# Optimization experiments

Measured on AMD Instinct MI355X. Metric: run time of the kernel, lower is better.

## Reference

```python
import jax, jax.numpy as jnp
import numpy as np

NUM_GROUPS = 16
EPS = 1e-6


def setup_inputs() -> dict:
    key = jax.random.key(0)
    ks = jax.random.split(key, 6)
    b, c, t, h, w = 2, 256, 4, 32, 32
    x = jax.random.normal(ks[0], (b, c, t, h, w), dtype=jnp.float32)
    scale = 0.02
    return {
        "x": x,
        "gamma": jnp.ones((c,), jnp.float32),
        "beta": jnp.zeros((c,), jnp.float32),
        "wq": jax.random.normal(ks[1], (c, c), jnp.float32) * scale,
        "bq": jnp.zeros((c,), jnp.float32),
        "wk": jax.random.normal(ks[2], (c, c), jnp.float32) * scale,
        "bk": jnp.zeros((c,), jnp.float32),
        "wv": jax.random.normal(ks[3], (c, c), jnp.float32) * scale,
        "bv": jnp.zeros((c,), jnp.float32),
        "wp": jax.random.normal(ks[4], (c, c), jnp.float32) * scale,
        "bp": jnp.zeros((c,), jnp.float32),
    }


def _group_norm(x, gamma, beta):
    b, c, t, h, w = x.shape
    xg = x.reshape(b, NUM_GROUPS, -1)  # [b, G, (c/G)*t*h*w]
    mu = jnp.mean(xg, axis=2, keepdims=True)
    var = jnp.var(xg, axis=2, keepdims=True)
    xn = ((xg - mu) * jax.lax.rsqrt(var + EPS)).reshape(b, c, t, h, w)
    return xn * gamma[None, :, None, None, None] + beta[None, :, None, None, None]


def reference(x, gamma, beta, wq, bq, wk, bk, wv, bv, wp, bp):
    b, c, t, h, w = x.shape
    n = t * h * w
    hn = _group_norm(x, gamma, beta).reshape(b, c, n)  # [b, c, n]
    # 1x1x1 conv == channel matmul
    q = jnp.einsum("oc,bcn->bon", wq, hn) + bq[None, :, None]
    k = jnp.einsum("oc,bcn->bon", wk, hn) + bk[None, :, None]
    v = jnp.einsum("oc,bcn->bon", wv, hn) + bv[None, :, None]
    # scores[b, i, j] = sum_c q[b,c,i] k[b,c,j] / sqrt(c)
    scores = jnp.einsum("bci,bcj->bij", q, k) * (float(c) ** -0.5)
    attn = jax.nn.softmax(scores, axis=2)  # [b, n, n]
    # h_[b, c, i] = sum_j v[b,c,j] attn[b,i,j]
    ho = jnp.einsum("bcj,bij->bci", v, attn)
    out = jnp.einsum("oc,bcn->bon", wp, ho) + bp[None, :, None]
    return x + out.reshape(b, c, t, h, w)
```

## Files before the change

### kernel.cpp

```cpp
#include <hip/hip_runtime.h>
#include <hip/hip_bf16.h>

#define NB 2
#define NC 256
#define NN 4096
#define NG 16
#define GSZ (16*NN)
#define SPLIT 4
#define SCL 0.09014205f

typedef __attribute__((ext_vector_type(8))) short bf16x8;
typedef __attribute__((ext_vector_type(4))) float f32x4;
typedef __attribute__((ext_vector_type(8))) unsigned short u16x8;

static __device__ __forceinline__ unsigned short f2b(float f) {
    union { float f; unsigned u; } x; x.f = f;
    unsigned r = x.u + 0x7fffu + ((x.u >> 16) & 1u);
    return (unsigned short)(r >> 16);
}
static __device__ __forceinline__ float b2f(unsigned short u) {
    union { unsigned u; float f; } x; x.u = ((unsigned)u) << 16;
    return x.f;
}
static __device__ __forceinline__ void glds16(const void* g, void* l) {
    __builtin_amdgcn_global_load_lds(
        (const __attribute__((address_space(1))) unsigned int*)g,
        (__attribute__((address_space(3))) unsigned int*)l, 16, 0, 0);
}

__global__ void k_wcvt(const float* __restrict__ wq, const float* __restrict__ wk,
                       const float* __restrict__ wv, const float* __restrict__ wp,
                       unsigned short* __restrict__ dst) {
    int idx = (blockIdx.x * 256 + threadIdx.x) * 4;
    int which = idx >> 16, off = idx & 65535;
    const float* s = (which == 0) ? wq : (which == 1) ? wk : (which == 2) ? wv : wp;
    float4 v = *(const float4*)(s + off);
    dst[idx + 0] = f2b(v.x);
    dst[idx + 1] = f2b(v.y);
    dst[idx + 2] = f2b(v.z);
    dst[idx + 3] = f2b(v.w);
}

__global__ void k_stats(const float* __restrict__ x, float* __restrict__ stats) {
    int bg = blockIdx.x >> 3, seg = blockIdx.x & 7;
    const float4* p = (const float4*)(x + (size_t)bg * GSZ + (size_t)seg * (GSZ / 8));
    float s1 = 0.f, s2 = 0.f;
    for (int k = threadIdx.x; k < GSZ / 8 / 4; k += 256) {
        float4 v = p[k];
        s1 += v.x + v.y + v.z + v.w;
        s2 += v.x*v.x + v.y*v.y + v.z*v.z + v.w*v.w;
    }
    #pragma unroll
    for (int m = 1; m < 64; m <<= 1) { s1 += __shfl_xor(s1, m); s2 += __shfl_xor(s2, m); }
    __shared__ float r1[4], r2[4];
    int w = threadIdx.x >> 6;
    if ((threadIdx.x & 63) == 0) { r1[w] = s1; r2[w] = s2; }
    __syncthreads();
    if (threadIdx.x == 0) {
        float a = 0.f, b = 0.f;
        #pragma unroll
        for (int i = 0; i < 4; i++) { a += r1[i]; b += r2[i]; }
        atomicAdd(&stats[bg * 2], a);
        atomicAdd(&stats[bg * 2 + 1], b);
    }
}

__global__ void k_norm_t(const float* __restrict__ x, const float* __restrict__ gamma,
                         const float* __restrict__ beta, const float* __restrict__ stats,
                         unsigned short* __restrict__ hn_t) {
    __shared__ unsigned short tile[64][66];
    int n0 = blockIdx.x * 64, c0 = blockIdx.y * 64, b = blockIdx.z;
    int cc = threadIdx.x >> 2, part = threadIdx.x & 3;
    int c = c0 + cc;
    float s1 = stats[(b * NG + (c >> 4)) * 2];
    float s2 = stats[(b * NG + (c >> 4)) * 2 + 1];
    float mean = s1 * (1.f / (float)GSZ);
    float var  = s2 * (1.f / (float)GSZ) - mean * mean;
    float rstd = rsqrtf(var + 1e-6f);
    float sc = rstd * gamma[c];
    float sh = beta[c] - mean * sc;
    const float4* row = (const float4*)(x + ((size_t)b * NC + c) * NN + n0);
    #pragma unroll
    for (int q = 0; q < 4; q++) {
        int f4 = part * 4 + q;
        float4 v = row[f4];
        tile[cc][f4*4+0] = f2b(v.x * sc + sh);
        tile[cc][f4*4+1] = f2b(v.y * sc + sh);
        tile[cc][f4*4+2] = f2b(v.z * sc + sh);
        tile[cc][f4*4+3] = f2b(v.w * sc + sh);
    }
    __syncthreads();
    int nn = threadIdx.x >> 2;
    u16x8 o0, o1;
    #pragma unroll
    for (int e = 0; e < 8; e++) { o0[e] = tile[part*16 + e][nn]; o1[e] = tile[part*16 + 8 + e][nn]; }
    unsigned short* dst = hn_t + ((size_t)b * NN + n0 + nn) * NC + c0 + part * 16;
    *(u16x8*)dst = o0;
    *(u16x8*)(dst + 8) = o1;
}

__global__ __launch_bounds__(256, 2) void k_qkv(
        const unsigned short* __restrict__ hn_t, const unsigned short* __restrict__ wb,
        const float* __restrict__ bq, const float* __restrict__ bk, const float* __restrict__ bv,
        unsigned short* __restrict__ q_t, unsigned short* __restrict__ k_t,
        unsigned short* __restrict__ v_cm) {
    int i0 = blockIdx.x * 64, which = blockIdx.y, b = blockIdx.z;
    int lane = threadIdx.x & 63, w = threadIdx.x >> 6;
    const unsigned short* W = wb + which * 65536;
    const float* bias = (which == 0) ? bq : (which == 1) ? bk : bv;
    if (which < 2) {
        const unsigned short* arow =
            hn_t + ((size_t)b * NN + i0 + w * 16 + (lane & 15)) * NC + ((lane >> 4) * 8);
        f32x4 acc[16];
        #pragma unroll
        for (int t = 0; t < 16; t++) acc[t] = (f32x4){0.f, 0.f, 0.f, 0.f};
        #pragma unroll
        for (int kk = 0; kk < 8; kk++) {
            bf16x8 af = *(const bf16x8*)(arow + kk * 32);
            const unsigned short* bbase = W + (size_t)(lane & 15) * NC + kk * 32 + ((lane >> 4) * 8);
            #pragma unroll
            for (int ot = 0; ot < 16; ot++) {
                bf16x8 bf_ = *(const bf16x8*)(bbase + (size_t)ot * 16 * NC);
                acc[ot] = __builtin_amdgcn_mfma_f32_16x16x32_bf16(af, bf_, acc[ot], 0, 0, 0);
            }
        }
        unsigned short* dst = ((which == 0) ? q_t : k_t) + (size_t)b * NN * NC;
        #pragma unroll
        for (int ot = 0; ot < 16; ot++) {
            float bv_ = bias[ot * 16 + (lane & 15)];
            #pragma unroll
            for (int r = 0; r < 4; r++) {
                int i = i0 + w * 16 + (lane >> 4) * 4 + r;
                dst[(size_t)i * NC + ot * 16 + (lane & 15)] = f2b(acc[ot][r] + bv_);
            }
        }
    } else {
        f32x4 acc[4][4];
        #pragma unroll
        for (int mt = 0; mt < 4; mt++)
            #pragma unroll
            for (int nt = 0; nt < 4; nt++) acc[mt][nt] = (f32x4){0.f, 0.f, 0.f, 0.f};
        #pragma unroll
        for (int kk = 0; kk < 8; kk++) {
            bf16x8 bfr[4];
            #pragma unroll
            for (int nt = 0; nt < 4; nt++)
                bfr[nt] = *(const bf16x8*)(hn_t + ((size_t)b * NN + i0 + nt * 16 + (lane & 15)) * NC
                                           + kk * 32 + ((lane >> 4) * 8));
            #pragma unroll
            for (int mt = 0; mt < 4; mt++) {
                bf16x8 af = *(const bf16x8*)(W + (size_t)(w * 64 + mt * 16 + (lane & 15)) * NC
                                             + kk * 32 + ((lane >> 4) * 8));
                #pragma unroll
                for (int nt = 0; nt < 4; nt++)
                    acc[mt][nt] = __builtin_amdgcn_mfma_f32_16x16x32_bf16(af, bfr[nt], acc[mt][nt], 0, 0, 0);
            }
        }
        #pragma unroll
        for (int mt = 0; mt < 4; mt++) {
            #pragma unroll
            for (int r = 0; r < 4; r++) {
                int o = w * 64 + mt * 16 + (lane >> 4) * 4 + r;
                float bv_ = bias[o];
                #pragma unroll
                for (int nt = 0; nt < 4; nt++) {
                    int i = i0 + nt * 16 + (lane & 15);
                    v_cm[(size_t)b * NC * NN + (size_t)o * NN + i] = f2b(acc[mt][nt][r] + bv_);
                }
            }
        }
    }
}

__global__ __launch_bounds__(512, 2) void k_attn(
        const unsigned short* __restrict__ q_t, const unsigned short* __restrict__ k_t,
        const unsigned short* __restrict__ v_cm,
        unsigned short* __restrict__ po, float* __restrict__ ml) {
    __shared__ __attribute__((aligned(16))) unsigned short Ks[2][16384];
    __shared__ __attribute__((aligned(16))) unsigned short Vs[2][16384];
    __shared__ __attribute__((aligned(16))) unsigned short Ps[8][1024];
    int d = blockIdx.x;
    int g = d & 7, xb = d >> 3;
    int sp = g & 3, b = g >> 2;
    int i0 = xb * 128;
    int lane = threadIdx.x & 63, w = threadIdx.x >> 6;
    size_t bO = (size_t)b * NN * NC;
    bf16x8 qf[8];
    {
        const unsigned short* qrow =
            q_t + bO + (size_t)(i0 + w * 16 + (lane & 15)) * NC + ((lane >> 4) * 8);
        #pragma unroll
        for (int kk = 0; kk < 8; kk++) qf[kk] = *(const bf16x8*)(qrow + kk * 32);
    }
    int j0b = sp * 1024;
    const char* gpk[4];
    const char* gpv[4];
    {
        const char* kbase = (const char*)(k_t + bO);
        const char* vbase = (const char*)(v_cm + bO);
        #pragma unroll
        for (int r = 0; r < 4; r++) {
            int jr = r * 16 + w * 2 + (lane >> 5);
            int cb = (lane & 31) * 16;
            gpk[r] = kbase + (size_t)(j0b + jr) * 512 + (cb ^ ((jr & 7) << 4));
            int cr = r * 64 + w * 8 + (lane >> 3);
            int jb = (lane & 7) * 16;
            gpv[r] = vbase + (size_t)cr * 8192 + (size_t)j0b * 2 + (jb ^ ((cr & 7) << 4));
        }
    }
    f32x4 o[16];
    #pragma unroll
    for (int t = 0; t < 16; t++) o[t] = (f32x4){0.f, 0.f, 0.f, 0.f};
    float m[4], l[4];
    #pragma unroll
    for (int r = 0; r < 4; r++) { m[r] = -1e30f; l[r] = 0.f; }
    #pragma unroll
    for (int r = 0; r < 4; r++) {
        glds16(gpk[r], (char*)&Ks[0][0] + w * 1024 + r * 8192);
        glds16(gpv[r], (char*)&Vs[0][0] + w * 1024 + r * 8192);
    }
    __syncthreads();
    int cur = 0;
    #pragma unroll 1
    for (int t = 0; t < 16; ++t) {
        if (t < 15) {
            #pragma unroll
            for (int r = 0; r < 4; r++) { gpk[r] += 32768; gpv[r] += 128; }
            int nb = cur ^ 1;
            #pragma unroll
            for (int r = 0; r < 4; r++) {
                glds16(gpk[r], (char*)&Ks[nb][0] + w * 1024 + r * 8192);
                glds16(gpv[r], (char*)&Vs[nb][0] + w * 1024 + r * 8192);
            }
        }
        const char* KsB = (const char*)&Ks[cur][0];
        const char* VsB = (const char*)&Vs[cur][0];
        f32x4 s[4];
        #pragma unroll
        for (int tt = 0; tt < 4; tt++) s[tt] = (f32x4){0.f, 0.f, 0.f, 0.f};
        #pragma unroll
        for (int kk = 0; kk < 8; kk++) {
            #pragma unroll
            for (int tt = 0; tt < 4; tt++) {
                unsigned off = ((unsigned)((tt * 16 + (lane & 15)) * 512 + kk * 64 + ((lane >> 4) * 16)))
                               ^ (((unsigned)(lane & 7)) << 4);
                bf16x8 kf = *(const bf16x8*)(KsB + off);
                s[tt] = __builtin_amdgcn_mfma_f32_16x16x32_bf16(qf[kk], kf, s[tt], 0, 0, 0);
            }
        }
        float corr[4];
        #pragma unroll
        for (int r = 0; r < 4; r++) {
            float v0 = fmaxf(fmaxf(s[0][r], s[1][r]), fmaxf(s[2][r], s[3][r]));
            v0 = fmaxf(v0, __shfl_xor(v0, 1));
            v0 = fmaxf(v0, __shfl_xor(v0, 2));
            v0 = fmaxf(v0, __shfl_xor(v0, 4));
            v0 = fmaxf(v0, __shfl_xor(v0, 8));
            float mn = fmaxf(m[r], v0);
            corr[r] = exp2f((m[r] - mn) * SCL);
            m[r] = mn;
        }
        float rs[4] = {0.f, 0.f, 0.f, 0.f};
        #pragma unroll
        for (int tt = 0; tt < 4; tt++) {
            #pragma unroll
            for (int r = 0; r < 4; r++) {
                float p = exp2f((s[tt][r] - m[r]) * SCL);
                rs[r] += p;
                unsigned i_ = (lane >> 4) * 4 + r;
                unsigned off = ((unsigned)(i_ * 128 + (tt * 16 + (lane & 15)) * 2)) ^ ((i_ & 7) << 4);
                *(unsigned short*)((char*)&Ps[w][0] + off) = f2b(p);
            }
        }
        #pragma unroll
        for (int r = 0; r < 4; r++) {
            float v0 = rs[r];
            v0 += __shfl_xor(v0, 1); v0 += __shfl_xor(v0, 2);
            v0 += __shfl_xor(v0, 4); v0 += __shfl_xor(v0, 8);
            l[r] = l[r] * corr[r] + v0;
        }
        #pragma unroll
        for (int tt = 0; tt < 16; tt++) {
            #pragma unroll
            for (int r = 0; r < 4; r++) o[tt][r] *= corr[r];
        }
        #pragma unroll
        for (int kk = 0; kk < 2; kk++) {
            unsigned offp = ((unsigned)((lane & 15) * 128 + kk * 64 + ((lane >> 4) * 16)))
                            ^ (((unsigned)(lane & 7)) << 4);
            bf16x8 pf = *(const bf16x8*)((char*)&Ps[w][0] + offp);
            #pragma unroll
            for (int ct = 0; ct < 16; ct++) {
                unsigned offv = ((unsigned)((ct * 16 + (lane & 15)) * 128 + kk * 64 + ((lane >> 4) * 16)))
                                ^ (((unsigned)(lane & 7)) << 4);
                bf16x8 vf = *(const bf16x8*)(VsB + offv);
                o[ct] = __builtin_amdgcn_mfma_f32_16x16x32_bf16(pf, vf, o[ct], 0, 0, 0);
            }
        }
        __syncthreads();
        cur ^= 1;
    }
    unsigned short* dst = po + ((size_t)(sp * NB + b) * NN) * NC;
    #pragma unroll
    for (int ct = 0; ct < 16; ct++) {
        #pragma unroll
        for (int r = 0; r < 4; r++) {
            int i = i0 + w * 16 + (lane >> 4) * 4 + r;
            dst[(size_t)i * NC + ct * 16 + (lane & 15)] = f2b(o[ct][r]);
        }
    }
    if ((lane & 15) == 0) {
        #pragma unroll
        for (int r = 0; r < 4; r++) {
            int i = i0 + w * 16 + (lane >> 4) * 4 + r;
            size_t mi = ((size_t)(sp * NB + b) * NN + i) * 2;
            ml[mi] = m[r];
            ml[mi + 1] = l[r];
        }
    }
}

__global__ void k_winv(const float* __restrict__ ml, float* __restrict__ winv) {
    int idx = blockIdx.x * 256 + threadIdx.x;
    float mv[SPLIT], lv[SPLIT];
    float M = -1e30f;
    #pragma unroll
    for (int s = 0; s < SPLIT; s++) {
        size_t mi = ((size_t)(s * 8192 + idx)) * 2;
        mv[s] = ml[mi]; lv[s] = ml[mi + 1];
        M = fmaxf(M, mv[s]);
    }
    float den = 0.f, wg[SPLIT];
    #pragma unroll
    for (int s = 0; s < SPLIT; s++) { wg[s] = exp2f((mv[s] - M) * SCL); den += wg[s] * lv[s]; }
    float inv = 1.f / den;
    #pragma unroll
    for (int s = 0; s < SPLIT; s++) winv[s * 8192 + idx] = wg[s] * inv;
}

__global__ __launch_bounds__(256, 4) void k_proj(
        const unsigned short* __restrict__ po, const float* __restrict__ winv,
        const unsigned short* __restrict__ wp_b, const float* __restrict__ bp,
        const float* __restrict__ x, float* __restrict__ out) {
    __shared__ __attribute__((aligned(16))) unsigned short Hs[32 * 256];
    int i0 = blockIdx.x * 32, b = blockIdx.y;
    int tid = threadIdx.x, lane = tid & 63, w = tid >> 6;
    {
        int il = tid >> 3, cq = tid & 7;
        int i = i0 + il;
        float wg[SPLIT];
        #pragma unroll
        for (int s = 0; s < SPLIT; s++) wg[s] = winv[s * 8192 + b * NN + i];
        #pragma unroll
        for (int e = 0; e < 4; e++) {
            float accv[8];
            #pragma unroll
            for (int q = 0; q < 8; q++) accv[q] = 0.f;
            #pragma unroll
            for (int s = 0; s < SPLIT; s++) {
                u16x8 v = *(const u16x8*)(po + ((size_t)(s * NB + b) * NN + i) * NC + cq * 32 + e * 8);
                #pragma unroll
                for (int q = 0; q < 8; q++) accv[q] += wg[s] * b2f(v[q]);
            }
            u16x8 rv;
            #pragma unroll
            for (int q = 0; q < 8; q++) rv[q] = f2b(accv[q]);
            unsigned off = ((unsigned)(il * 512 + cq * 64 + e * 16)) ^ ((il & 7) << 4);
            *(u16x8*)((char*)Hs + off) = rv;
        }
    }
    __syncthreads();
    f32x4 acc[4][2];
    #pragma unroll
    for (int mt = 0; mt < 4; mt++)
        #pragma unroll
        for (int nt = 0; nt < 2; nt++) acc[mt][nt] = (f32x4){0.f, 0.f, 0.f, 0.f};
    #pragma unroll
    for (int kk = 0; kk < 8; kk++) {
        bf16x8 bfr[2];
        #pragma unroll
        for (int nt = 0; nt < 2; nt++) {
            unsigned off = ((unsigned)((nt * 16 + (lane & 15)) * 512 + kk * 64 + ((lane >> 4) * 16)))
                           ^ (((unsigned)(lane & 7)) << 4);
            bfr[nt] = *(const bf16x8*)((char*)Hs + off);
        }
        #pragma unroll
        for (int mt = 0; mt < 4; mt++) {
            bf16x8 af = *(const bf16x8*)(wp_b + (size_t)(w * 64 + mt * 16 + (lane & 15)) * NC
                                         + kk * 32 + ((lane >> 4) * 8));
            #pragma unroll
            for (int nt = 0; nt < 2; nt++)
                acc[mt][nt] = __builtin_amdgcn_mfma_f32_16x16x32_bf16(af, bfr[nt], acc[mt][nt], 0, 0, 0);
        }
    }
    #pragma unroll
    for (int mt = 0; mt < 4; mt++) {
        #pragma unroll
        for (int r = 0; r < 4; r++) {
            int o = w * 64 + mt * 16 + (lane >> 4) * 4 + r;
            float bv_ = bp[o];
            #pragma unroll
            for (int nt = 0; nt < 2; nt++) {
                int i = i0 + nt * 16 + (lane & 15);
                size_t idx = ((size_t)b * NC + o) * NN + i;
                out[idx] = x[idx] + acc[mt][nt][r] + bv_;
            }
        }
    }
}

extern "C" void kernel_launch(void* const* d_in, const int* in_sizes, int n_in,
                              void* d_out, int out_size, void* d_ws, size_t ws_size,
                              hipStream_t stream) {
    const float* x     = (const float*)d_in[0];
    const float* gamma = (const float*)d_in[1];
    const float* beta  = (const float*)d_in[2];
    const float* wq    = (const float*)d_in[3];
    const float* bq    = (const float*)d_in[4];
    const float* wk    = (const float*)d_in[5];
    const float* bk    = (const float*)d_in[6];
    const float* wv    = (const float*)d_in[7];
    const float* bv    = (const float*)d_in[8];
    const float* wp    = (const float*)d_in[9];
    const float* bp    = (const float*)d_in[10];
    float* out = (float*)d_out;

    char* ws = (char*)d_ws;
    const size_t SZ_T = (size_t)NB * NN * NC * 2;
    float*          stats = (float*)ws;
    unsigned short* wb    = (unsigned short*)(ws + 1024);
    unsigned short* hn_t  = (unsigned short*)(ws + 1024 + 524288);
    unsigned short* q_t   = (unsigned short*)((char*)hn_t + SZ_T);
    unsigned short* k_t   = (unsigned short*)((char*)q_t + SZ_T);
    unsigned short* v_cm  = (unsigned short*)((char*)k_t + SZ_T);
    unsigned short* po    = (unsigned short*)((char*)v_cm + SZ_T);
    float*          ml    = (float*)((char*)po + (size_t)SPLIT * SZ_T);
    float*          winv  = (float*)((char*)ml + 262144);

    hipMemsetAsync(stats, 0, 1024, stream);
    k_wcvt<<<256, 256, 0, stream>>>(wq, wk, wv, wp, wb);
    k_stats<<<256, 256, 0, stream>>>(x, stats);
    k_norm_t<<<dim3(NN / 64, NC / 64, NB), 256, 0, stream>>>(x, gamma, beta, stats, hn_t);
    k_qkv<<<dim3(NN / 64, 3, NB), 256, 0, stream>>>(hn_t, wb, bq, bk, bv, q_t, k_t, v_cm);
    k_attn<<<256, 512, 0, stream>>>(q_t, k_t, v_cm, po, ml);
    k_winv<<<32, 256, 0, stream>>>(ml, winv);
    k_proj<<<dim3(NN / 32, NB), 256, 0, stream>>>(po, winv, wb + 3 * 65536, bp, x, out);
}
```

Before: 216.0 us.

## Double query rows per attention wave, split keys 8-way, lazy softmax rescale, fuse combine

Each attention wave now handles two 16-row query tiles, so every K/V fragment read from LDS feeds twice as many MFMAs. The key range is split eight ways, which keeps 256 blocks. The online softmax only rescales the output accumulators when the running max grows past a threshold, skipping most of the per-tile correction multiplies. The separate k_winv kernel is folded into k_proj, which removes one launch, and the workspace is repacked so po aliases hn_t. The added cost is twice as many accumulator registers (risk of spills or lower occupancy) and a larger split-combine step in k_proj; s_setprio hints are also added around the MFMA sections.

```diff
diff --git a/kernel.cpp b/kernel.cpp
--- a/kernel.cpp
+++ b/kernel.cpp
@@ -6,8 +6,10 @@
 #define NN 4096
 #define NG 16
 #define GSZ (16*NN)
-#define SPLIT 4
+#define SPLIT 8
+#define JT (NN / SPLIT / 64)
 #define SCL 0.09014205f
+#define THRRAW 88.0f
 
 typedef __attribute__((ext_vector_type(8))) short bf16x8;
 typedef __attribute__((ext_vector_type(4))) float f32x4;
@@ -99,7 +101,7 @@
     *(u16x8*)(dst + 8) = o1;
 }
 
-__global__ __launch_bounds__(256, 2) void k_qkv(
+__global__ __launch_bounds__(256, 4) void k_qkv(
         const unsigned short* __restrict__ hn_t, const unsigned short* __restrict__ wb,
         const float* __restrict__ bq, const float* __restrict__ bk, const float* __restrict__ bv,
         unsigned short* __restrict__ q_t, unsigned short* __restrict__ k_t,
@@ -178,66 +180,66 @@
         unsigned short* __restrict__ po, float* __restrict__ ml) {
     __shared__ __attribute__((aligned(16))) unsigned short Ks[2][16384];
     __shared__ __attribute__((aligned(16))) unsigned short Vs[2][16384];
-    __shared__ __attribute__((aligned(16))) unsigned short Ps[8][1024];
-    int d = blockIdx.x;
-    int g = d & 7, xb = d >> 3;
-    int sp = g & 3, b = g >> 2;
-    int i0 = xb * 128;
+    __shared__ __attribute__((aligned(16))) unsigned short Ps[8][2048];
+    int bid = blockIdx.x;
+    int sp = bid & 7, b = (bid >> 3) & 1, xb = bid >> 4;
+    int i0 = xb * 256;
     int lane = threadIdx.x & 63, w = threadIdx.x >> 6;
     size_t bO = (size_t)b * NN * NC;
-    bf16x8 qf[8];
-    {
+    bf16x8 qf[2][8];
+    #pragma unroll
+    for (int h = 0; h < 2; h++) {
         const unsigned short* qrow =
-            q_t + bO + (size_t)(i0 + w * 16 + (lane & 15)) * NC + ((lane >> 4) * 8);
-        #pragma unroll
-        for (int kk = 0; kk < 8; kk++) qf[kk] = *(const bf16x8*)(qrow + kk * 32);
-    }
-    int j0b = sp * 1024;
-    const char* gpk[4];
-    const char* gpv[4];
-    {
-        const char* kbase = (const char*)(k_t + bO);
-        const char* vbase = (const char*)(v_cm + bO);
-        #pragma unroll
-        for (int r = 0; r < 4; r++) {
-            int jr = r * 16 + w * 2 + (lane >> 5);
-            int cb = (lane & 31) * 16;
-            gpk[r] = kbase + (size_t)(j0b + jr) * 512 + (cb ^ ((jr & 7) << 4));
-            int cr = r * 64 + w * 8 + (lane >> 3);
-            int jb = (lane & 7) * 16;
-            gpv[r] = vbase + (size_t)cr * 8192 + (size_t)j0b * 2 + (jb ^ ((cr & 7) << 4));
-        }
-    }
-    f32x4 o[16];
-    #pragma unroll
-    for (int t = 0; t < 16; t++) o[t] = (f32x4){0.f, 0.f, 0.f, 0.f};
-    float m[4], l[4];
-    #pragma unroll
-    for (int r = 0; r < 4; r++) { m[r] = -1e30f; l[r] = 0.f; }
+            q_t + bO + (size_t)(i0 + w * 32 + h * 16 + (lane & 15)) * NC + ((lane >> 4) * 8);
+        #pragma unroll
+        for (int kk = 0; kk < 8; kk++) qf[h][kk] = *(const bf16x8*)(qrow + kk * 32);
+    }
+    unsigned kstat[4], vstat[4];
     #pragma unroll
     for (int r = 0; r < 4; r++) {
-        glds16(gpk[r], (char*)&Ks[0][0] + w * 1024 + r * 8192);
-        glds16(gpv[r], (char*)&Vs[0][0] + w * 1024 + r * 8192);
+        int jr = r * 16 + w * 2 + (lane >> 5);
+        kstat[r] = (unsigned)(jr * 512 + (((lane & 31) * 16) ^ ((jr & 7) << 4)));
+        int cr = r * 64 + w * 8 + (lane >> 3);
+        vstat[r] = (unsigned)(cr * 8192 + (((lane & 7) * 16) ^ ((cr & 7) << 4)));
+    }
+    const char* kp = (const char*)(k_t + bO) + (size_t)sp * 262144;
+    const char* vp = (const char*)(v_cm + bO) + (size_t)sp * 1024;
+    f32x4 o[2][16];
+    #pragma unroll
+    for (int h = 0; h < 2; h++)
+        #pragma unroll
+        for (int t = 0; t < 16; t++) o[h][t] = (f32x4){0.f, 0.f, 0.f, 0.f};
+    float m[2][4], l[2][4];
+    #pragma unroll
+    for (int h = 0; h < 2; h++)
+        #pragma unroll
+        for (int r = 0; r < 4; r++) { m[h][r] = -1e30f; l[h][r] = 0.f; }
+    #pragma unroll
+    for (int r = 0; r < 4; r++) {
+        glds16(kp + kstat[r], (char*)&Ks[0][0] + w * 1024 + r * 8192);
+        glds16(vp + vstat[r], (char*)&Vs[0][0] + w * 1024 + r * 8192);
     }
     __syncthreads();
     int cur = 0;
     #pragma unroll 1
-    for (int t = 0; t < 16; ++t) {
-        if (t < 15) {
-            #pragma unroll
-            for (int r = 0; r < 4; r++) { gpk[r] += 32768; gpv[r] += 128; }
+    for (int t = 0; t < JT; ++t) {
+        if (t < JT - 1) {
+            kp += 32768; vp += 128;
             int nb = cur ^ 1;
             #pragma unroll
             for (int r = 0; r < 4; r++) {
-                glds16(gpk[r], (char*)&Ks[nb][0] + w * 1024 + r * 8192);
-                glds16(gpv[r], (char*)&Vs[nb][0] + w * 1024 + r * 8192);
+                glds16(kp + kstat[r], (char*)&Ks[nb][0] + w * 1024 + r * 8192);
+                glds16(vp + vstat[r], (char*)&Vs[nb][0] + w * 1024 + r * 8192);
             }
         }
         const char* KsB = (const char*)&Ks[cur][0];
         const char* VsB = (const char*)&Vs[cur][0];
-        f32x4 s[4];
-        #pragma unroll
-        for (int tt = 0; tt < 4; tt++) s[tt] = (f32x4){0.f, 0.f, 0.f, 0.f};
+        f32x4 s[2][4];
+        #pragma unroll
+        for (int h = 0; h < 2; h++)
+            #pragma unroll
+            for (int tt = 0; tt < 4; tt++) s[h][tt] = (f32x4){0.f, 0.f, 0.f, 0.f};
+        __builtin_amdgcn_s_setprio(1);
         #pragma unroll
         for (int kk = 0; kk < 8; kk++) {
             #pragma unroll
@@ -245,101 +247,109 @@
                 unsigned off = ((unsigned)((tt * 16 + (lane & 15)) * 512 + kk * 64 + ((lane >> 4) * 16)))
                                ^ (((unsigned)(lane & 7)) << 4);
                 bf16x8 kf = *(const bf16x8*)(KsB + off);
-                s[tt] = __builtin_amdgcn_mfma_f32_16x16x32_bf16(qf[kk], kf, s[tt], 0, 0, 0);
-            }
-        }
-        float corr[4];
-        #pragma unroll
-        for (int r = 0; r < 4; r++) {
-            float v0 = fmaxf(fmaxf(s[0][r], s[1][r]), fmaxf(s[2][r], s[3][r]));
-            v0 = fmaxf(v0, __shfl_xor(v0, 1));
-            v0 = fmaxf(v0, __shfl_xor(v0, 2));
-            v0 = fmaxf(v0, __shfl_xor(v0, 4));
-            v0 = fmaxf(v0, __shfl_xor(v0, 8));
-            float mn = fmaxf(m[r], v0);
-            corr[r] = exp2f((m[r] - mn) * SCL);
-            m[r] = mn;
-        }
-        float rs[4] = {0.f, 0.f, 0.f, 0.f};
-        #pragma unroll
-        for (int tt = 0; tt < 4; tt++) {
-            #pragma unroll
-            for (int r = 0; r < 4; r++) {
-                float p = exp2f((s[tt][r] - m[r]) * SCL);
-                rs[r] += p;
-                unsigned i_ = (lane >> 4) * 4 + r;
-                unsigned off = ((unsigned)(i_ * 128 + (tt * 16 + (lane & 15)) * 2)) ^ ((i_ & 7) << 4);
-                *(unsigned short*)((char*)&Ps[w][0] + off) = f2b(p);
-            }
-        }
-        #pragma unroll
-        for (int r = 0; r < 4; r++) {
-            float v0 = rs[r];
-            v0 += __shfl_xor(v0, 1); v0 += __shfl_xor(v0, 2);
-            v0 += __shfl_xor(v0, 4); v0 += __shfl_xor(v0, 8);
-            l[r] = l[r] * corr[r] + v0;
-        }
-        #pragma unroll
-        for (int tt = 0; tt < 16; tt++) {
-            #pragma unroll
-            for (int r = 0; r < 4; r++) o[tt][r] *= corr[r];
-        }
+                s[0][tt] = __builtin_amdgcn_mfma_f32_16x16x32_bf16(qf[0][kk], kf, s[0][tt], 0, 0, 0);
+                s[1][tt] = __builtin_amdgcn_mfma_f32_16x16x32_bf16(qf[1][kk], kf, s[1][tt], 0, 0, 0);
+            }
+        }
+        __builtin_amdgcn_s_setprio(0);
+        #pragma unroll
+        for (int h = 0; h < 2; h++) {
+            float vmax[4];
+            #pragma unroll
+            for (int r = 0; r < 4; r++) {
+                float v0 = fmaxf(fmaxf(s[h][0][r], s[h][1][r]), fmaxf(s[h][2][r], s[h][3][r]));
+                v0 = fmaxf(v0, __shfl_xor(v0, 1));
+                v0 = fmaxf(v0, __shfl_xor(v0, 2));
+                v0 = fmaxf(v0, __shfl_xor(v0, 4));
+                v0 = fmaxf(v0, __shfl_xor(v0, 8));
+                vmax[r] = v0;
+            }
+            float tmax = fmaxf(fmaxf(vmax[0] - m[h][0], vmax[1] - m[h][1]),
+                               fmaxf(vmax[2] - m[h][2], vmax[3] - m[h][3]));
+            tmax = fmaxf(tmax, __shfl_xor(tmax, 16));
+            tmax = fmaxf(tmax, __shfl_xor(tmax, 32));
+            if (tmax > THRRAW) {
+                #pragma unroll
+                for (int r = 0; r < 4; r++) {
+                    float mn = fmaxf(m[h][r], vmax[r]);
+                    float corr = exp2f((m[h][r] - mn) * SCL);
+                    m[h][r] = mn;
+                    l[h][r] *= corr;
+                    #pragma unroll
+                    for (int ct = 0; ct < 16; ct++) o[h][ct][r] *= corr;
+                }
+            }
+            float rs[4] = {0.f, 0.f, 0.f, 0.f};
+            #pragma unroll
+            for (int tt = 0; tt < 4; tt++) {
+                #pragma unroll
+                for (int r = 0; r < 4; r++) {
+                    float p = exp2f((s[h][tt][r] - m[h][r]) * SCL);
+                    rs[r] += p;
+                    unsigned i_ = (unsigned)(h * 16 + (lane >> 4) * 4 + r);
+                    unsigned off = ((unsigned)(i_ * 128 + (tt * 16 + (lane & 15)) * 2)) ^ ((i_ & 7) << 4);
+                    *(unsigned short*)((char*)&Ps[w][0] + off) = f2b(p);
+                }
+            }
+            #pragma unroll
+            for (int r = 0; r < 4; r++) {
+                float v0 = rs[r];
+                v0 += __shfl_xor(v0, 1); v0 += __shfl_xor(v0, 2);
+                v0 += __shfl_xor(v0, 4); v0 += __shfl_xor(v0, 8);
+                l[h][r] += v0;
+            }
+        }
+        __builtin_amdgcn_s_setprio(1);
         #pragma unroll
         for (int kk = 0; kk < 2; kk++) {
-            unsigned offp = ((unsigned)((lane & 15) * 128 + kk * 64 + ((lane >> 4) * 16)))
-                            ^ (((unsigned)(lane & 7)) << 4);
-            bf16x8 pf = *(const bf16x8*)((char*)&Ps[w][0] + offp);
+            bf16x8 pf[2];
+            #pragma unroll
+            for (int h = 0; h < 2; h++) {
+                unsigned row = (unsigned)(h * 16 + (lane & 15));
+                unsigned offp = ((unsigned)(row * 128 + kk * 64 + ((lane >> 4) * 16))) ^ ((row & 7) << 4);
+                pf[h] = *(const bf16x8*)((char*)&Ps[w][0] + offp);
+            }
             #pragma unroll
             for (int ct = 0; ct < 16; ct++) {
                 unsigned offv = ((unsigned)((ct * 16 + (lane & 15)) * 128 + kk * 64 + ((lane >> 4) * 16)))
                                 ^ (((unsigned)(lane & 7)) << 4);
                 bf16x8 vf = *(const bf16x8*)(VsB + offv);
-                o[ct] = __builtin_amdgcn_mfma_f32_16x16x32_bf16(pf, vf, o[ct], 0, 0, 0);
-            }
-        }
+                o[0][ct] = __builtin_amdgcn_mfma_f32_16x16x32_bf16(pf[0], vf, o[0][ct], 0, 0, 0);
+                o[1][ct] = __builtin_amdgcn_mfma_f32_16x16x32_bf16(pf[1], vf, o[1][ct], 0, 0, 0);
+            }
+        }
+        __builtin_amdgcn_s_setprio(0);
         __syncthreads();
         cur ^= 1;
     }
-    unsigned short* dst = po + ((size_t)(sp * NB + b) * NN) * NC;
-    #pragma unroll
-    for (int ct = 0; ct < 16; ct++) {
-        #pragma unroll
-        for (int r = 0; r < 4; r++) {
-            int i = i0 + w * 16 + (lane >> 4) * 4 + r;
-            dst[(size_t)i * NC + ct * 16 + (lane & 15)] = f2b(o[ct][r]);
+    unsigned short* dst = po + (size_t)(sp * NB + b) * NN * NC;
+    #pragma unroll
+    for (int h = 0; h < 2; h++) {
+        #pragma unroll
+        for (int ct = 0; ct < 16; ct++) {
+            #pragma unroll
+            for (int r = 0; r < 4; r++) {
+                int i = i0 + w * 32 + h * 16 + (lane >> 4) * 4 + r;
+                dst[(size_t)i * NC + ct * 16 + (lane & 15)] = f2b(o[h][ct][r]);
+            }
         }
     }
     if ((lane & 15) == 0) {
         #pragma unroll
-        for (int r = 0; r < 4; r++) {
-            int i = i0 + w * 16 + (lane >> 4) * 4 + r;
-            size_t mi = ((size_t)(sp * NB + b) * NN + i) * 2;
-            ml[mi] = m[r];
-            ml[mi + 1] = l[r];
-        }
-    }
-}
-
-__global__ void k_winv(const float* __restrict__ ml, float* __restrict__ winv) {
-    int idx = blockIdx.x * 256 + threadIdx.x;
-    float mv[SPLIT], lv[SPLIT];
-    float M = -1e30f;
-    #pragma unroll
-    for (int s = 0; s < SPLIT; s++) {
-        size_t mi = ((size_t)(s * 8192 + idx)) * 2;
-        mv[s] = ml[mi]; lv[s] = ml[mi + 1];
-        M = fmaxf(M, mv[s]);
-    }
-    float den = 0.f, wg[SPLIT];
-    #pragma unroll
-    for (int s = 0; s < SPLIT; s++) { wg[s] = exp2f((mv[s] - M) * SCL); den += wg[s] * lv[s]; }
-    float inv = 1.f / den;
-    #pragma unroll
-    for (int s = 0; s < SPLIT; s++) winv[s * 8192 + idx] = wg[s] * inv;
+        for (int h = 0; h < 2; h++) {
+            #pragma unroll
+            for (int r = 0; r < 4; r++) {
+                int i = i0 + w * 32 + h * 16 + (lane >> 4) * 4 + r;
+                size_t mi = ((size_t)(sp * NB + b) * NN + i) * 2;
+                ml[mi] = m[h][r];
+                ml[mi + 1] = l[h][r];
+            }
+        }
+    }
 }
 
 __global__ __launch_bounds__(256, 4) void k_proj(
-        const unsigned short* __restrict__ po, const float* __restrict__ winv,
+        const unsigned short* __restrict__ po, const float* __restrict__ ml,
         const unsigned short* __restrict__ wp_b, const float* __restrict__ bp,
         const float* __restrict__ x, float* __restrict__ out) {
     __shared__ __attribute__((aligned(16))) unsigned short Hs[32 * 256];
@@ -348,9 +358,20 @@
     {
         int il = tid >> 3, cq = tid & 7;
         int i = i0 + il;
-        float wg[SPLIT];
-        #pragma unroll
-        for (int s = 0; s < SPLIT; s++) wg[s] = winv[s * 8192 + b * NN + i];
+        float mv[SPLIT], lv[SPLIT];
+        float M = -1e30f;
+        #pragma unroll
+        for (int s = 0; s < SPLIT; s++) {
+            size_t mi = ((size_t)(s * NB + b) * NN + i) * 2;
+            mv[s] = ml[mi]; lv[s] = ml[mi + 1];
+            M = fmaxf(M, mv[s]);
+        }
+        float den = 0.f, wg[SPLIT];
+        #pragma unroll
+        for (int s = 0; s < SPLIT; s++) { wg[s] = exp2f((mv[s] - M) * SCL); den += wg[s] * lv[s]; }
+        float inv = 1.f / den;
+        #pragma unroll
+        for (int s = 0; s < SPLIT; s++) wg[s] *= inv;
         #pragma unroll
         for (int e = 0; e < 4; e++) {
             float accv[8];
@@ -426,16 +447,15 @@
     float* out = (float*)d_out;
 
     char* ws = (char*)d_ws;
-    const size_t SZ_T = (size_t)NB * NN * NC * 2;
+    const size_t MB = 1024 * 1024;
     float*          stats = (float*)ws;
     unsigned short* wb    = (unsigned short*)(ws + 1024);
-    unsigned short* hn_t  = (unsigned short*)(ws + 1024 + 524288);
-    unsigned short* q_t   = (unsigned short*)((char*)hn_t + SZ_T);
-    unsigned short* k_t   = (unsigned short*)((char*)q_t + SZ_T);
-    unsigned short* v_cm  = (unsigned short*)((char*)k_t + SZ_T);
-    unsigned short* po    = (unsigned short*)((char*)v_cm + SZ_T);
-    float*          ml    = (float*)((char*)po + (size_t)SPLIT * SZ_T);
-    float*          winv  = (float*)((char*)ml + 262144);
+    unsigned short* q_t   = (unsigned short*)(ws + 1 * MB);
+    unsigned short* k_t   = (unsigned short*)(ws + 5 * MB);
+    unsigned short* v_cm  = (unsigned short*)(ws + 9 * MB);
+    float*          ml    = (float*)(ws + 13 * MB);
+    unsigned short* hn_t  = (unsigned short*)(ws + 14 * MB);
+    unsigned short* po    = (unsigned short*)(ws + 14 * MB);
 
     hipMemsetAsync(stats, 0, 1024, stream);
     k_wcvt<<<256, 256, 0, stream>>>(wq, wk, wv, wp, wb);
@@ -443,6 +463,5 @@
     k_norm_t<<<dim3(NN / 64, NC / 64, NB), 256, 0, stream>>>(x, gamma, beta, stats, hn_t);
     k_qkv<<<dim3(NN / 64, 3, NB), 256, 0, stream>>>(hn_t, wb, bq, bk, bv, q_t, k_t, v_cm);
     k_attn<<<256, 512, 0, stream>>>(q_t, k_t, v_cm, po, ml);
-    k_winv<<<32, 256, 0, stream>>>(ml, winv);
-    k_proj<<<dim3(NN / 32, NB), 256, 0, stream>>>(po, winv, wb + 3 * 65536, bp, x, out);
-}
+    k_proj<<<dim3(NN / 32, NB), 256, 0, stream>>>(po, ml, wb + 3 * 65536, bp, x, out);
+}
```

Result: slower. 403.9 us (+87.0%).
